# Performance work log

Measured on AMD Instinct MI355X. Metric: run time of the kernel, lower is better.

The kernel has to match this reference:

```python
import jax, jax.numpy as jnp
import numpy as np

SR = 44100
S_TAUS = [10.0, 50.0, 100.0]   # ms
L_TAUS = [500.0, 1500.0, 3000.0]  # ms
EPS = 1e-8


def ms2coef(ms, sr):
    return float(1.0 - np.exp(-2200.0 / (ms * sr)))


def ema(x, coef):
    # First-order leaky integrator y[t] = coef*x[t] + (1-coef)*y[t-1], y[-1]=0.
    # x: [B, T]; scan over time with carry of shape [B].
    coef = jnp.asarray(coef, x.dtype)
    one_m = jnp.asarray(1.0, x.dtype) - coef

    def step(carry, xt):
        y = coef * xt + one_m * carry
        return y, y

    _, ys = jax.lax.scan(step, jnp.zeros(x.shape[0], x.dtype), x.T)
    return ys.T  # [B, T]


def hadamard(x):
    # mid/side transform on channel dim (-2), orthonormal scaling
    m = x[..., 0, :] + x[..., 1, :]
    s = x[..., 0, :] - x[..., 1, :]
    return jnp.stack([m, s], axis=-2) * jnp.asarray(np.sqrt(0.5), x.dtype)


def ldr_feat(x_sq, s_coef, l_coef, shift):
    # log short-term envelope minus (time-aligned) log long-term envelope
    short = jnp.log(ema(x_sq, s_coef))
    long_ = jnp.log(ema(x_sq, l_coef))
    return short - jnp.roll(long_, -shift, axis=-1)


def setup_inputs() -> dict:
    key = jax.random.key(0)
    k1, k2 = jax.random.split(key)
    x_pred = jax.random.normal(k1, (4, 2, 1048576), dtype=jnp.float32)
    x_true = jax.random.normal(k2, (4, 2, 1048576), dtype=jnp.float32)
    return {"x_pred": x_pred, "x_true": x_true}


def reference(x_pred, x_true):
    xp = hadamard(x_pred)
    xt = hadamard(x_true)
    T = xp.shape[-1]
    ps = jnp.clip(jnp.square(xp), EPS, None).reshape(-1, T)
    ts = jnp.clip(jnp.square(xt), EPS, None).reshape(-1, T)
    total = jnp.asarray(0.0, x_pred.dtype)
    for s_ms, l_ms in zip(S_TAUS, L_TAUS):
        sc = ms2coef(s_ms, SR)
        lc = ms2coef(l_ms, SR)
        shift = int(SR * (l_ms - s_ms) * 0.0005)
        fp = ldr_feat(ps, sc, lc, shift)
        ft = ldr_feat(ts, sc, lc, shift)
        total = total + jnp.mean(jnp.abs(fp - ft))
    return total
```

## Files before the change

### kernel.cpp

```cpp
#include <hip/hip_runtime.h>
#include <cmath>


#define T_LEN    1048576
#define CHUNKS   256
#define CLEN     4096
#define NT1      256
#define SEG1     16
#define COLS     65536
#define JMAX     65535
#define EPS_CLIP 1e-8f
#define K2SEG    32
#define K2NSEG   8

struct K1Args {
  float d[6];
  float apw[6][7];
};
struct K2Args {
  float dL[6];
  float dL32[6];
};
struct CarryPack {
  float d[3];
  float apw[3][9];
};

__device__ __constant__ const int D_SHIFT[3] = {10804, 31972, 63945};

__global__ __launch_bounds__(NT1)
void k1_stage(const float* __restrict__ xp, const float* __restrict__ xt,
              float* __restrict__ Eloc, float* __restrict__ Bs,
              float* __restrict__ Bl, int mode, K1Args ka)
{
  int chunk = blockIdx.x, b = blockIdx.y;
  int which = b >> 2, sig = b & 3, tid = threadIdx.x;
  long base = (long)chunk * CLEN + (long)tid * SEG1;
  const float* x0 = (which ? xt : xp) + (long)sig * 2 * T_LEN;
  const float* x1 = x0 + T_LEN;

  float S[12];
#pragma unroll
  for (int j = 0; j < 12; j++) S[j] = 0.f;

#pragma unroll
  for (int i = 0; i < SEG1 / 4; i++) {
    float4 a = *(const float4*)(x0 + base + 4*i);
    float4 c4 = *(const float4*)(x1 + base + 4*i);
    float sm, sp, pm, ps;
#define STEP(CMP) \
    sm = a.CMP + c4.CMP; sp = a.CMP - c4.CMP; \
    pm = fmaxf(0.5f * sm * sm, EPS_CLIP); ps = fmaxf(0.5f * sp * sp, EPS_CLIP); \
    _Pragma("unroll") \
    for (int cf = 0; cf < 6; cf++) { \
      S[cf*2+0] = fmaf(ka.d[cf], S[cf*2+0], pm); \
      S[cf*2+1] = fmaf(ka.d[cf], S[cf*2+1], ps); \
    }
    STEP(x) STEP(y) STEP(z) STEP(w)
#undef STEP
  }

  int lane = tid & 63, w = tid >> 6;
#pragma unroll
  for (int i = 0; i < 6; i++) {
#pragma unroll
    for (int j = 0; j < 12; j++) {
      float up = __shfl_up(S[j], 1u << i, 64);
      if (lane >= (1 << i)) S[j] = fmaf(ka.apw[j >> 1][i], up, S[j]);
    }
  }
  __shared__ float WT[4][12];
  if (lane == 63)
#pragma unroll
    for (int j = 0; j < 12; j++) WT[w][j] = S[j];
  __syncthreads();
  float C[12];
#pragma unroll
  for (int j = 0; j < 12; j++) C[j] = 0.f;
#pragma unroll
  for (int i = 0; i < 4; i++) {
    if (i < w) {
#pragma unroll
      for (int j = 0; j < 12; j++)
        C[j] = fmaf(ka.apw[j >> 1][6], C[j], WT[i][j]);
    }
  }
  float alp[6];
#pragma unroll
  for (int cf = 0; cf < 6; cf++) {
    int e = lane + 1;
    float a = 1.f;
#pragma unroll
    for (int i = 0; i < 7; i++)
      if (e & (1 << i)) a *= ka.apw[cf][i];
    alp[cf] = a;
  }
#pragma unroll
  for (int j = 0; j < 12; j++) S[j] = fmaf(alp[j >> 1], C[j], S[j]);

  long col = (long)chunk * (CLEN / SEG1) + tid;
  if (mode & 2) {
#pragma unroll
    for (int k = 0; k < 3; k++)
#pragma unroll
      for (int st2 = 0; st2 < 2; st2++)
        Bs[(long)(4*k + which*2 + st2) * (4L*COLS) + (long)sig*COLS + col] = S[4*k + st2];
  }
  if (mode & 1) {
#pragma unroll
    for (int k = 0; k < 3; k++)
#pragma unroll
      for (int st2 = 0; st2 < 2; st2++)
        Bl[(long)(4*k + which*2 + st2) * (4L*COLS) + (long)sig*COLS + col] = S[4*k + 2 + st2];
  }
  if (mode != 2 && tid == NT1 - 1) {
#pragma unroll
    for (int cf = 0; cf < 6; cf++)
#pragma unroll
      for (int st = 0; st < 2; st++)
        Eloc[chunk * 96 + (which*8 + sig*2 + st) * 6 + cf] = S[cf*2 + st];
  }
}

__global__ __launch_bounds__(768)
void k2_scan(const float* __restrict__ Eloc, float* __restrict__ Y, K2Args ka,
             float* __restrict__ out)
{
  int col = threadIdx.x;
  int seg = threadIdx.y;
  if (col == 0 && seg == 0) out[0] = 0.f;
  float dL = ka.dL[col % 6];
  float A  = ka.dL32[col % 6];
  int c0 = seg * K2SEG;

  float yloc[K2SEG];
  float y = 0.f;
#pragma unroll
  for (int i = 0; i < K2SEG; i++) {
    y = fmaf(dL, y, Eloc[(c0 + i) * 96 + col]);
    yloc[i] = y;
  }
  __shared__ float SY[K2NSEG][96];
  SY[seg][col] = y;
  __syncthreads();
  float C = 0.f;
  for (int s = 0; s < seg; s++) C = fmaf(A, C, SY[s][col]);
  float w = dL;
#pragma unroll
  for (int i = 0; i < K2SEG; i++) {
    Y[(c0 + i) * 96 + col] = fmaf(w, C, yloc[i]);
    w *= dL;
  }
}

__global__ __launch_bounds__(256)
void k3_table(const float* __restrict__ Bl, const float* __restrict__ Y,
              float* __restrict__ Etab, CarryPack cp)
{
  int chunk = blockIdx.x, sig = blockIdx.y, tid = threadIdx.x;
  long col = (long)chunk * 256 + tid;

  float Yc[12];
#pragma unroll
  for (int j = 0; j < 12; j++) Yc[j] = 0.f;
  if (chunk > 0) {
    const float* Yp = Y + (chunk - 1) * 96;
    int rm = sig * 2;
#pragma unroll
    for (int k = 0; k < 3; k++) {
      int cf = 2*k + 1;
      Yc[4*k+0] = Yp[rm*6 + cf];       Yc[4*k+1] = Yp[(rm+1)*6 + cf];
      Yc[4*k+2] = Yp[(8+rm)*6 + cf];   Yc[4*k+3] = Yp[(8+rm+1)*6 + cf];
    }
  }
  float fac[3];
#pragma unroll
  for (int k = 0; k < 3; k++) {
    int e = tid + 1;
    float a = 1.f;
#pragma unroll
    for (int i = 0; i < 9; i++)
      if (e & (1 << i)) a *= cp.apw[k][i];
    fac[k] = a;
  }
#pragma unroll
  for (int k = 0; k < 3; k++) {
    float y0 = fmaf(fac[k], Yc[4*k+0], Bl[(long)(4*k+0)*(4L*COLS) + (long)sig*COLS + col]);
    float y1 = fmaf(fac[k], Yc[4*k+1], Bl[(long)(4*k+1)*(4L*COLS) + (long)sig*COLS + col]);
    float y2 = fmaf(fac[k], Yc[4*k+2], Bl[(long)(4*k+2)*(4L*COLS) + (long)sig*COLS + col]);
    float y3 = fmaf(fac[k], Yc[4*k+3], Bl[(long)(4*k+3)*(4L*COLS) + (long)sig*COLS + col]);
    float em = __log2f(y0) - __log2f(y2);
    float es = __log2f(y1) - __log2f(y3);
    long rowm = (long)(k*8 + sig*2);
    Etab[rowm * COLS + col] = em;
    Etab[(rowm+1) * COLS + col] = es;
  }
}

__global__ __launch_bounds__(256)
void k4all(const float* __restrict__ xp, const float* __restrict__ xt,
           const float* __restrict__ Y, const float* __restrict__ Bs,
           const float* __restrict__ Etab, CarryPack cp, float* __restrict__ out)
{
  int chunk = blockIdx.x, sig = blockIdx.y, tid = threadIdx.x;
  long col = (long)chunk * 256 + tid;
  long base = col * 16;

  float Yc[12];
#pragma unroll
  for (int j = 0; j < 12; j++) Yc[j] = 0.f;
  if (chunk > 0) {
    const float* Yp = Y + (chunk - 1) * 96;
    int rm = sig * 2;
#pragma unroll
    for (int k = 0; k < 3; k++) {
      int cf = 2*k;
      Yc[4*k+0] = Yp[rm*6 + cf];       Yc[4*k+1] = Yp[(rm+1)*6 + cf];
      Yc[4*k+2] = Yp[(8+rm)*6 + cf];   Yc[4*k+3] = Yp[(8+rm+1)*6 + cf];
    }
  }
  float y[12];
  if (tid == 0) {
#pragma unroll
    for (int j = 0; j < 12; j++) y[j] = Yc[j];
  } else {
    float fac[3];
#pragma unroll
    for (int k = 0; k < 3; k++) {
      float a = 1.f;
#pragma unroll
      for (int i = 0; i < 8; i++)
        if (tid & (1 << i)) a *= cp.apw[k][i];
      fac[k] = a;
    }
#pragma unroll
    for (int k = 0; k < 3; k++)
#pragma unroll
      for (int q = 0; q < 4; q++)
        y[4*k+q] = fmaf(fac[k], Yc[4*k+q],
                        Bs[(long)(4*k+q)*(4L*COLS) + (long)sig*COLS + (col-1)]);
  }

  float tm0[3], tm1[3], tm2[3], ts0[3], ts1[3], ts2[3];
  int ofs[3];
#pragma unroll
  for (int k = 0; k < 3; k++) {
    int q0 = (int)base + D_SHIFT[k]; if (q0 >= T_LEN) q0 -= T_LEN;
    int qc = q0 - 15;
    qc = qc < 0 ? 0 : qc;
    const int QCAP = ((JMAX - 2) << 4) + 15;
    qc = qc > QCAP ? QCAP : qc;
    int j0 = qc >> 4;
    ofs[k] = qc & 15;
    const float* Tm = Etab + (long)(k * 8 + sig * 2) * COLS;
    const float* Ts = Tm + COLS;
    tm0[k] = Tm[j0]; tm1[k] = Tm[j0 + 1]; tm2[k] = Tm[j0 + 2];
    ts0[k] = Ts[j0]; ts1[k] = Ts[j0 + 1]; ts2[k] = Ts[j0 + 2];
  }

  const float* p0 = xp + (long)sig * 2 * T_LEN;
  const float* p1 = p0 + T_LEN;
  const float* t0 = xt + (long)sig * 2 * T_LEN;
  const float* t1 = t0 + T_LEN;

  float acc0 = 0.f, acc1 = 0.f;
#pragma unroll
  for (int qt = 0; qt < 4; qt++) {
    float4 a4 = *(const float4*)(p0 + base + 4*qt);
    float4 b4 = *(const float4*)(p1 + base + 4*qt);
    float4 u4 = *(const float4*)(t0 + base + 4*qt);
    float4 w4 = *(const float4*)(t1 + base + 4*qt);
#define SAMP(CI, CMP) { \
      const int m = 4*qt + CI; \
      float sm = a4.CMP + b4.CMP, sd = a4.CMP - b4.CMP; \
      float pm = fmaxf(0.5f*sm*sm, EPS_CLIP), ps = fmaxf(0.5f*sd*sd, EPS_CLIP); \
      float em_ = u4.CMP + w4.CMP, ed_ = u4.CMP - w4.CMP; \
      float qm_ = fmaxf(0.5f*em_*em_, EPS_CLIP), qs_ = fmaxf(0.5f*ed_*ed_, EPS_CLIP); \
      _Pragma("unroll") \
      for (int k = 0; k < 3; k++) { \
        float dd = cp.d[k]; \
        y[4*k+0] = fmaf(dd, y[4*k+0], pm);  y[4*k+1] = fmaf(dd, y[4*k+1], ps); \
        y[4*k+2] = fmaf(dd, y[4*k+2], qm_); y[4*k+3] = fmaf(dd, y[4*k+3], qs_); \
        float Dm = __log2f(y[4*k+0]) - __log2f(y[4*k+2]); \
        float Ds = __log2f(y[4*k+1]) - __log2f(y[4*k+3]); \
        int d0 = ofs[k] + m; \
        bool hi = d0 >= 16; \
        float am = hi ? tm1[k] : tm0[k], bm = hi ? tm2[k] : tm1[k]; \
        float as = hi ? ts1[k] : ts0[k], bs = hi ? ts2[k] : ts1[k]; \
        float f = (float)(d0 - (hi ? 16 : 0)) * 0.0625f; \
        float em = fmaf(f, bm - am, am); \
        float es = fmaf(f, bs - as, as); \
        acc0 += fabsf(Dm - em); \
        acc1 += fabsf(Ds - es); \
      } \
    }
    SAMP(0,x) SAMP(1,y) SAMP(2,z) SAMP(3,w)
#undef SAMP
  }

  float acc = acc0 + acc1;
#pragma unroll
  for (int off = 32; off > 0; off >>= 1) acc += __shfl_down(acc, off, 64);
  __shared__ float psum[4];
  int lane = tid & 63, w = tid >> 6;
  if (lane == 0) psum[w] = acc;
  __syncthreads();
  if (tid == 0) {
    const float SCALE = (float)(0.6931471805599453 / (8.0 * 1048576.0));
    float s = psum[0] + psum[1] + psum[2] + psum[3];
    atomicAdd(out, s * SCALE);
  }
}

extern "C" void kernel_launch(void* const* d_in, const int* in_sizes, int n_in,
                              void* d_out, int out_size, void* d_ws, size_t ws_size,
                              hipStream_t stream)
{
  (void)in_sizes; (void)n_in; (void)out_size;
  const float* xp = (const float*)d_in[0];
  const float* xt = (const float*)d_in[1];
  float* out = (float*)d_out;
  char* ws = (char*)d_ws;

  const size_t OFF_ELOC = 0;
  const size_t OFF_Y    = 98304;
  const size_t OFF_ETAB = 212992;
  const size_t OFF_B    = 6504448;
  const size_t HALF_B   = 12L * 4 * COLS * 4;
  const size_t NEED_FULL = OFF_B + 2 * HALF_B;
  float* Eloc = (float*)(ws + OFF_ELOC);
  float* Ybuf = (float*)(ws + OFF_Y);
  float* Etab = (float*)(ws + OFF_ETAB);
  float* Bsh  = (float*)(ws + OFF_B);
  float* Blo  = (float*)(ws + OFF_B + HALF_B);

  static const double S_MS[3] = {10.0, 50.0, 100.0};
  static const double L_MS[3] = {500.0, 1500.0, 3000.0};

  K1Args k1a; K2Args k2a; CarryPack cpS, cpL;
  for (int k = 0; k < 3; k++) {
    for (int which = 0; which < 2; which++) {
      int idx = 2 * k + which;
      double ms = which ? L_MS[k] : S_MS[k];
      float cF = (float)(1.0 - std::exp(-2200.0 / (ms * 44100.0)));
      float dF = 1.0f - cF;
      k1a.d[idx] = dF;
      double a16 = std::pow((double)dF, 16.0);
      for (int i = 0; i < 7; i++)
        k1a.apw[idx][i] = (float)std::pow(a16, (double)(1 << i));
      k2a.dL[idx]   = (float)std::pow((double)dF, (double)CLEN);
      k2a.dL32[idx] = (float)std::pow((double)dF, (double)CLEN * (double)K2SEG);
      CarryPack& cp = which ? cpL : cpS;
      cp.d[k] = dF;
      for (int i = 0; i < 9; i++)
        cp.apw[k][i] = (float)std::pow(a16, (double)(1 << i));
    }
  }

  bool full = (ws_size >= NEED_FULL);
  if (full) {
    k1_stage<<<dim3(CHUNKS, 8), NT1, 0, stream>>>(xp, xt, Eloc, Bsh, Blo, 3, k1a);
    k2_scan<<<dim3(1), dim3(96, K2NSEG), 0, stream>>>(Eloc, Ybuf, k2a, out);
    k3_table<<<dim3(CHUNKS, 4), 256, 0, stream>>>(Blo, Ybuf, Etab, cpL);
    k4all<<<dim3(CHUNKS, 4), 256, 0, stream>>>(xp, xt, Ybuf, Bsh, Etab, cpS, out);
  } else {
    k1_stage<<<dim3(CHUNKS, 8), NT1, 0, stream>>>(xp, xt, Eloc, Bsh, Bsh, 1, k1a);
    k2_scan<<<dim3(1), dim3(96, K2NSEG), 0, stream>>>(Eloc, Ybuf, k2a, out);
    k3_table<<<dim3(CHUNKS, 4), 256, 0, stream>>>(Bsh, Ybuf, Etab, cpL);
    k1_stage<<<dim3(CHUNKS, 8), NT1, 0, stream>>>(xp, xt, Eloc, Bsh, Bsh, 2, k1a);
    k4all<<<dim3(CHUNKS, 4), 256, 0, stream>>>(xp, xt, Ybuf, Bsh, Etab, cpS, out);
  }
}
```

Baseline: 136.3 us.

## Halve k4all per-thread segment to 8 samples using mid-segment short-EMA carries

k1_stage now also emits the short-envelope state at the midpoint of each 16-sample segment. It reconstructs this from a pre-midpoint snapshot and the shuffled exclusive prefix, then writes it interleaved with the end-of-segment state into a doubled B8 buffer. k4all then launches twice as many blocks, each thread processing 8 samples instead of 16, with carry factors recomputed for a d^8 stride. The aim is to double parallelism in the serial, log-heavy final pass and shorten each thread's dependency chain. In exchange, k1 writes more carry state and does extra shuffles and arithmetic, and k4 re-reads more Etab and carry data per sample.

```diff
diff --git a/kernel.cpp b/kernel.cpp
--- a/kernel.cpp
+++ b/kernel.cpp
@@ -16,6 +16,7 @@
 struct K1Args {
   float d[6];
   float apw[6][7];
+  float a8[6];
 };
 struct K2Args {
   float dL[6];
@@ -30,7 +31,7 @@
 
 __global__ __launch_bounds__(NT1)
 void k1_stage(const float* __restrict__ xp, const float* __restrict__ xt,
-              float* __restrict__ Eloc, float* __restrict__ Bs,
+              float* __restrict__ Eloc, float* __restrict__ B8,
               float* __restrict__ Bl, int mode, K1Args ka)
 {
   int chunk = blockIdx.x, b = blockIdx.y;
@@ -42,9 +43,14 @@
   float S[12];
 #pragma unroll
   for (int j = 0; j < 12; j++) S[j] = 0.f;
+  float S8[6];
 
 #pragma unroll
   for (int i = 0; i < SEG1 / 4; i++) {
+    if (i == 2) {
+#pragma unroll
+      for (int k = 0; k < 3; k++) { S8[2*k] = S[4*k]; S8[2*k+1] = S[4*k+1]; }
+    }
     float4 a = *(const float4*)(x0 + base + 4*i);
     float4 c4 = *(const float4*)(x1 + base + 4*i);
     float sm, sp, pm, ps;
@@ -69,6 +75,15 @@
       if (lane >= (1 << i)) S[j] = fmaf(ka.apw[j >> 1][i], up, S[j]);
     }
   }
+  float X8[6];
+#pragma unroll
+  for (int k = 0; k < 3; k++) {
+#pragma unroll
+    for (int st = 0; st < 2; st++) {
+      float xv = __shfl_up(S[4*k+st], 1, 64);
+      X8[2*k+st] = (lane == 0) ? 0.f : xv;
+    }
+  }
   __shared__ float WT[4][12];
   if (lane == 63)
 #pragma unroll
@@ -95,16 +110,32 @@
       if (e & (1 << i)) a *= ka.apw[cf][i];
     alp[cf] = a;
   }
+  float alpE[3];
+#pragma unroll
+  for (int k = 0; k < 3; k++) {
+    float a = 1.f;
+#pragma unroll
+    for (int i = 0; i < 6; i++)
+      if (lane & (1 << i)) a *= ka.apw[2*k][i];
+    alpE[k] = a;
+  }
 #pragma unroll
   for (int j = 0; j < 12; j++) S[j] = fmaf(alp[j >> 1], C[j], S[j]);
 
   long col = (long)chunk * (CLEN / SEG1) + tid;
   if (mode & 2) {
-#pragma unroll
-    for (int k = 0; k < 3; k++)
-#pragma unroll
-      for (int st2 = 0; st2 < 2; st2++)
-        Bs[(long)(4*k + which*2 + st2) * (4L*COLS) + (long)sig*COLS + col] = S[4*k + st2];
+    long col2 = col * 2;
+#pragma unroll
+    for (int k = 0; k < 3; k++) {
+#pragma unroll
+      for (int st = 0; st < 2; st++) {
+        float E   = fmaf(alpE[k], C[4*k+st], X8[2*k+st]);
+        float mid = fmaf(ka.a8[2*k], E, S8[2*k+st]);
+        long row = 4*k + which*2 + st;
+        *(float2*)(B8 + row*(8L*COLS) + (long)sig*(2L*COLS) + col2)
+            = make_float2(mid, S[4*k+st]);
+      }
+    }
   }
   if (mode & 1) {
 #pragma unroll
@@ -199,12 +230,13 @@
 
 __global__ __launch_bounds__(256)
 void k4all(const float* __restrict__ xp, const float* __restrict__ xt,
-           const float* __restrict__ Y, const float* __restrict__ Bs,
+           const float* __restrict__ Y, const float* __restrict__ B8,
            const float* __restrict__ Etab, CarryPack cp, float* __restrict__ out)
 {
-  int chunk = blockIdx.x, sig = blockIdx.y, tid = threadIdx.x;
-  long col = (long)chunk * 256 + tid;
-  long base = col * 16;
+  int hb = blockIdx.x, sig = blockIdx.y, tid = threadIdx.x;
+  int chunk = hb >> 1;
+  int hc = ((hb & 1) << 8) + tid;
+  long s0 = ((long)chunk * 512 + hc) * 8;
 
   float Yc[12];
 #pragma unroll
@@ -220,7 +252,7 @@
     }
   }
   float y[12];
-  if (tid == 0) {
+  if (hc == 0) {
 #pragma unroll
     for (int j = 0; j < 12; j++) y[j] = Yc[j];
   } else {
@@ -229,23 +261,24 @@
     for (int k = 0; k < 3; k++) {
       float a = 1.f;
 #pragma unroll
-      for (int i = 0; i < 8; i++)
-        if (tid & (1 << i)) a *= cp.apw[k][i];
+      for (int i = 0; i < 9; i++)
+        if (hc & (1 << i)) a *= cp.apw[k][i];
       fac[k] = a;
     }
+    long g = (long)chunk * 512 + hc - 1;
 #pragma unroll
     for (int k = 0; k < 3; k++)
 #pragma unroll
       for (int q = 0; q < 4; q++)
         y[4*k+q] = fmaf(fac[k], Yc[4*k+q],
-                        Bs[(long)(4*k+q)*(4L*COLS) + (long)sig*COLS + (col-1)]);
+                        B8[(long)(4*k+q)*(8L*COLS) + (long)sig*(2L*COLS) + g]);
   }
 
   float tm0[3], tm1[3], tm2[3], ts0[3], ts1[3], ts2[3];
   int ofs[3];
 #pragma unroll
   for (int k = 0; k < 3; k++) {
-    int q0 = (int)base + D_SHIFT[k]; if (q0 >= T_LEN) q0 -= T_LEN;
+    int q0 = (int)s0 + D_SHIFT[k]; if (q0 >= T_LEN) q0 -= T_LEN;
     int qc = q0 - 15;
     qc = qc < 0 ? 0 : qc;
     const int QCAP = ((JMAX - 2) << 4) + 15;
@@ -265,11 +298,11 @@
 
   float acc0 = 0.f, acc1 = 0.f;
 #pragma unroll
-  for (int qt = 0; qt < 4; qt++) {
-    float4 a4 = *(const float4*)(p0 + base + 4*qt);
-    float4 b4 = *(const float4*)(p1 + base + 4*qt);
-    float4 u4 = *(const float4*)(t0 + base + 4*qt);
-    float4 w4 = *(const float4*)(t1 + base + 4*qt);
+  for (int qt = 0; qt < 2; qt++) {
+    float4 a4 = *(const float4*)(p0 + s0 + 4*qt);
+    float4 b4 = *(const float4*)(p1 + s0 + 4*qt);
+    float4 u4 = *(const float4*)(t0 + s0 + 4*qt);
+    float4 w4 = *(const float4*)(t1 + s0 + 4*qt);
 #define SAMP(CI, CMP) { \
       const int m = 4*qt + CI; \
       float sm = a4.CMP + b4.CMP, sd = a4.CMP - b4.CMP; \
@@ -325,14 +358,16 @@
   const size_t OFF_ELOC = 0;
   const size_t OFF_Y    = 98304;
   const size_t OFF_ETAB = 212992;
-  const size_t OFF_B    = 6504448;
-  const size_t HALF_B   = 12L * 4 * COLS * 4;
-  const size_t NEED_FULL = OFF_B + 2 * HALF_B;
+  const size_t OFF_B8   = 6504448;
+  const size_t B8_SZ    = 12L * 4 * 2 * COLS * 4;
+  const size_t OFF_BL   = OFF_B8 + B8_SZ;
+  const size_t BL_SZ    = 12L * 4 * COLS * 4;
+  const size_t NEED_FULL = OFF_BL + BL_SZ;
   float* Eloc = (float*)(ws + OFF_ELOC);
   float* Ybuf = (float*)(ws + OFF_Y);
   float* Etab = (float*)(ws + OFF_ETAB);
-  float* Bsh  = (float*)(ws + OFF_B);
-  float* Blo  = (float*)(ws + OFF_B + HALF_B);
+  float* B8   = (float*)(ws + OFF_B8);
+  float* Blo  = (float*)(ws + OFF_BL);
 
   static const double S_MS[3] = {10.0, 50.0, 100.0};
   static const double L_MS[3] = {500.0, 1500.0, 3000.0};
@@ -348,26 +383,29 @@
       double a16 = std::pow((double)dF, 16.0);
       for (int i = 0; i < 7; i++)
         k1a.apw[idx][i] = (float)std::pow(a16, (double)(1 << i));
+      k1a.a8[idx] = (float)std::pow((double)dF, 8.0);
       k2a.dL[idx]   = (float)std::pow((double)dF, (double)CLEN);
       k2a.dL32[idx] = (float)std::pow((double)dF, (double)CLEN * (double)K2SEG);
       CarryPack& cp = which ? cpL : cpS;
       cp.d[k] = dF;
+      double aS = which ? a16 : std::pow((double)dF, 8.0);
       for (int i = 0; i < 9; i++)
-        cp.apw[k][i] = (float)std::pow(a16, (double)(1 << i));
+        cp.apw[k][i] = (float)std::pow(aS, (double)(1 << i));
     }
   }
 
   bool full = (ws_size >= NEED_FULL);
   if (full) {
-    k1_stage<<<dim3(CHUNKS, 8), NT1, 0, stream>>>(xp, xt, Eloc, Bsh, Blo, 3, k1a);
+    k1_stage<<<dim3(CHUNKS, 8), NT1, 0, stream>>>(xp, xt, Eloc, B8, Blo, 3, k1a);
     k2_scan<<<dim3(1), dim3(96, K2NSEG), 0, stream>>>(Eloc, Ybuf, k2a, out);
     k3_table<<<dim3(CHUNKS, 4), 256, 0, stream>>>(Blo, Ybuf, Etab, cpL);
-    k4all<<<dim3(CHUNKS, 4), 256, 0, stream>>>(xp, xt, Ybuf, Bsh, Etab, cpS, out);
+    k4all<<<dim3(2*CHUNKS, 4), 256, 0, stream>>>(xp, xt, Ybuf, B8, Etab, cpS, out);
   } else {
-    k1_stage<<<dim3(CHUNKS, 8), NT1, 0, stream>>>(xp, xt, Eloc, Bsh, Bsh, 1, k1a);
+    float* BlA = (float*)(ws + OFF_B8);
+    k1_stage<<<dim3(CHUNKS, 8), NT1, 0, stream>>>(xp, xt, Eloc, B8, BlA, 1, k1a);
     k2_scan<<<dim3(1), dim3(96, K2NSEG), 0, stream>>>(Eloc, Ybuf, k2a, out);
-    k3_table<<<dim3(CHUNKS, 4), 256, 0, stream>>>(Bsh, Ybuf, Etab, cpL);
-    k1_stage<<<dim3(CHUNKS, 8), NT1, 0, stream>>>(xp, xt, Eloc, Bsh, Bsh, 2, k1a);
-    k4all<<<dim3(CHUNKS, 4), 256, 0, stream>>>(xp, xt, Ybuf, Bsh, Etab, cpS, out);
+    k3_table<<<dim3(CHUNKS, 4), 256, 0, stream>>>(BlA, Ybuf, Etab, cpL);
+    k1_stage<<<dim3(CHUNKS, 8), NT1, 0, stream>>>(xp, xt, Eloc, B8, BlA, 2, k1a);
+    k4all<<<dim3(2*CHUNKS, 4), 256, 0, stream>>>(xp, xt, Ybuf, B8, Etab, cpS, out);
   }
 }
```

Result: slower. 151.2 us (+10.9%).

## Fuse long-envelope table build into final loss kernel

Applied to the files above, without the earlier changes.

In the full-workspace path, the separate k3_table launch is removed and a new k4fused kernel rebuilds the needed long-term log-envelope values directly from the block-level state and carries. This drops one kernel launch and the write plus re-read of the Etab table. In exchange, each thread recomputes 3 table entries per tau, with extra logs and scattered Bl/Y reads, and neighbouring threads repeat overlapping work. The original kernel is renamed k4tab and stays in use for the fallback path.

```diff
diff --git a/kernel.cpp b/kernel.cpp
--- a/kernel.cpp
+++ b/kernel.cpp
@@ -198,7 +198,7 @@
 }
 
 __global__ __launch_bounds__(256)
-void k4all(const float* __restrict__ xp, const float* __restrict__ xt,
+void k4tab(const float* __restrict__ xp, const float* __restrict__ xt,
            const float* __restrict__ Y, const float* __restrict__ Bs,
            const float* __restrict__ Etab, CarryPack cp, float* __restrict__ out)
 {
@@ -312,6 +312,146 @@
   }
 }
 
+__global__ __launch_bounds__(256)
+void k4fused(const float* __restrict__ xp, const float* __restrict__ xt,
+             const float* __restrict__ Y, const float* __restrict__ Bs,
+             const float* __restrict__ Bl, CarryPack cpS, CarryPack cpL,
+             float* __restrict__ out)
+{
+  int chunk = blockIdx.x, sig = blockIdx.y, tid = threadIdx.x;
+  long col = (long)chunk * 256 + tid;
+  long base = col * 16;
+
+  float Yc[12];
+#pragma unroll
+  for (int j = 0; j < 12; j++) Yc[j] = 0.f;
+  if (chunk > 0) {
+    const float* Yp = Y + (chunk - 1) * 96;
+    int rm = sig * 2;
+#pragma unroll
+    for (int k = 0; k < 3; k++) {
+      int cf = 2*k;
+      Yc[4*k+0] = Yp[rm*6 + cf];       Yc[4*k+1] = Yp[(rm+1)*6 + cf];
+      Yc[4*k+2] = Yp[(8+rm)*6 + cf];   Yc[4*k+3] = Yp[(8+rm+1)*6 + cf];
+    }
+  }
+  float y[12];
+  if (tid == 0) {
+#pragma unroll
+    for (int j = 0; j < 12; j++) y[j] = Yc[j];
+  } else {
+    float fac[3];
+#pragma unroll
+    for (int k = 0; k < 3; k++) {
+      float a = 1.f;
+#pragma unroll
+      for (int i = 0; i < 8; i++)
+        if (tid & (1 << i)) a *= cpS.apw[k][i];
+      fac[k] = a;
+    }
+#pragma unroll
+    for (int k = 0; k < 3; k++)
+#pragma unroll
+      for (int q = 0; q < 4; q++)
+        y[4*k+q] = fmaf(fac[k], Yc[4*k+q],
+                        Bs[(long)(4*k+q)*(4L*COLS) + (long)sig*COLS + (col-1)]);
+  }
+
+  float tm0[3], tm1[3], tm2[3], ts0[3], ts1[3], ts2[3];
+  int ofs[3];
+#pragma unroll
+  for (int k = 0; k < 3; k++) {
+    int q0 = (int)base + D_SHIFT[k]; if (q0 >= T_LEN) q0 -= T_LEN;
+    int qc = q0 - 15;
+    qc = qc < 0 ? 0 : qc;
+    const int QCAP = ((JMAX - 2) << 4) + 15;
+    qc = qc > QCAP ? QCAP : qc;
+    int j0 = qc >> 4;
+    ofs[k] = qc & 15;
+    int cf = 2*k + 1;
+    float tmv[3], tsv[3];
+#pragma unroll
+    for (int p = 0; p < 3; p++) {
+      int g = j0 + p;
+      int ch = g >> 8, tp = g & 255;
+      float Y0 = 0.f, Y1 = 0.f, Y2 = 0.f, Y3 = 0.f;
+      if (ch > 0) {
+        const float* Yp = Y + (ch - 1) * 96;
+        int rm = sig * 2;
+        Y0 = Yp[rm*6 + cf];       Y1 = Yp[(rm+1)*6 + cf];
+        Y2 = Yp[(8+rm)*6 + cf];   Y3 = Yp[(8+rm+1)*6 + cf];
+      }
+      int e = tp + 1;
+      float a = 1.f;
+#pragma unroll
+      for (int i = 0; i < 9; i++)
+        if (e & (1 << i)) a *= cpL.apw[k][i];
+      long bg = (long)sig * COLS + g;
+      float w0 = fmaf(a, Y0, Bl[(long)(4*k+0)*(4L*COLS) + bg]);
+      float w1 = fmaf(a, Y1, Bl[(long)(4*k+1)*(4L*COLS) + bg]);
+      float w2 = fmaf(a, Y2, Bl[(long)(4*k+2)*(4L*COLS) + bg]);
+      float w3 = fmaf(a, Y3, Bl[(long)(4*k+3)*(4L*COLS) + bg]);
+      tmv[p] = __log2f(w0) - __log2f(w2);
+      tsv[p] = __log2f(w1) - __log2f(w3);
+    }
+    tm0[k] = tmv[0]; tm1[k] = tmv[1]; tm2[k] = tmv[2];
+    ts0[k] = tsv[0]; ts1[k] = tsv[1]; ts2[k] = tsv[2];
+  }
+
+  const float* p0 = xp + (long)sig * 2 * T_LEN;
+  const float* p1 = p0 + T_LEN;
+  const float* t0 = xt + (long)sig * 2 * T_LEN;
+  const float* t1 = t0 + T_LEN;
+
+  float acc0 = 0.f, acc1 = 0.f;
+#pragma unroll
+  for (int qt = 0; qt < 4; qt++) {
+    float4 a4 = *(const float4*)(p0 + base + 4*qt);
+    float4 b4 = *(const float4*)(p1 + base + 4*qt);
+    float4 u4 = *(const float4*)(t0 + base + 4*qt);
+    float4 w4 = *(const float4*)(t1 + base + 4*qt);
+#define SAMP(CI, CMP) { \
+      const int m = 4*qt + CI; \
+      float sm = a4.CMP + b4.CMP, sd = a4.CMP - b4.CMP; \
+      float pm = fmaxf(0.5f*sm*sm, EPS_CLIP), ps = fmaxf(0.5f*sd*sd, EPS_CLIP); \
+      float em_ = u4.CMP + w4.CMP, ed_ = u4.CMP - w4.CMP; \
+      float qm_ = fmaxf(0.5f*em_*em_, EPS_CLIP), qs_ = fmaxf(0.5f*ed_*ed_, EPS_CLIP); \
+      _Pragma("unroll") \
+      for (int k = 0; k < 3; k++) { \
+        float dd = cpS.d[k]; \
+        y[4*k+0] = fmaf(dd, y[4*k+0], pm);  y[4*k+1] = fmaf(dd, y[4*k+1], ps); \
+        y[4*k+2] = fmaf(dd, y[4*k+2], qm_); y[4*k+3] = fmaf(dd, y[4*k+3], qs_); \
+        float Dm = __log2f(y[4*k+0]) - __log2f(y[4*k+2]); \
+        float Ds = __log2f(y[4*k+1]) - __log2f(y[4*k+3]); \
+        int d0 = ofs[k] + m; \
+        bool hi = d0 >= 16; \
+        float am = hi ? tm1[k] : tm0[k], bm = hi ? tm2[k] : tm1[k]; \
+        float as = hi ? ts1[k] : ts0[k], bs = hi ? ts2[k] : ts1[k]; \
+        float f = (float)(d0 - (hi ? 16 : 0)) * 0.0625f; \
+        float em = fmaf(f, bm - am, am); \
+        float es = fmaf(f, bs - as, as); \
+        acc0 += fabsf(Dm - em); \
+        acc1 += fabsf(Ds - es); \
+      } \
+    }
+    SAMP(0,x) SAMP(1,y) SAMP(2,z) SAMP(3,w)
+#undef SAMP
+  }
+
+  float acc = acc0 + acc1;
+#pragma unroll
+  for (int off = 32; off > 0; off >>= 1) acc += __shfl_down(acc, off, 64);
+  __shared__ float psum[4];
+  int lane = tid & 63, w = tid >> 6;
+  if (lane == 0) psum[w] = acc;
+  __syncthreads();
+  if (tid == 0) {
+    const float SCALE = (float)(0.6931471805599453 / (8.0 * 1048576.0));
+    float s = psum[0] + psum[1] + psum[2] + psum[3];
+    atomicAdd(out, s * SCALE);
+  }
+}
+
 extern "C" void kernel_launch(void* const* d_in, const int* in_sizes, int n_in,
                               void* d_out, int out_size, void* d_ws, size_t ws_size,
                               hipStream_t stream)
@@ -361,13 +501,13 @@
   if (full) {
     k1_stage<<<dim3(CHUNKS, 8), NT1, 0, stream>>>(xp, xt, Eloc, Bsh, Blo, 3, k1a);
     k2_scan<<<dim3(1), dim3(96, K2NSEG), 0, stream>>>(Eloc, Ybuf, k2a, out);
-    k3_table<<<dim3(CHUNKS, 4), 256, 0, stream>>>(Blo, Ybuf, Etab, cpL);
-    k4all<<<dim3(CHUNKS, 4), 256, 0, stream>>>(xp, xt, Ybuf, Bsh, Etab, cpS, out);
+    k4fused<<<dim3(CHUNKS, 4), 256, 0, stream>>>(xp, xt, Ybuf, Bsh, Blo,
+                                                 cpS, cpL, out);
   } else {
     k1_stage<<<dim3(CHUNKS, 8), NT1, 0, stream>>>(xp, xt, Eloc, Bsh, Bsh, 1, k1a);
     k2_scan<<<dim3(1), dim3(96, K2NSEG), 0, stream>>>(Eloc, Ybuf, k2a, out);
     k3_table<<<dim3(CHUNKS, 4), 256, 0, stream>>>(Bsh, Ybuf, Etab, cpL);
     k1_stage<<<dim3(CHUNKS, 8), NT1, 0, stream>>>(xp, xt, Eloc, Bsh, Bsh, 2, k1a);
-    k4all<<<dim3(CHUNKS, 4), 256, 0, stream>>>(xp, xt, Ybuf, Bsh, Etab, cpS, out);
+    k4tab<<<dim3(CHUNKS, 4), 256, 0, stream>>>(xp, xt, Ybuf, Bsh, Etab, cpS, out);
   }
 }
```

New measurement: 131.0 us. 1.04x faster.
